# Kernel tuning notes

Hardware: AMD Instinct MI355X
Metric: run time of the kernel (lower is better)

## Reference

```python
import jax, jax.numpy as jnp
import numpy as np

N_BLOCKS = 500000
BLOCK_DIM = 64


def setup_inputs() -> dict:
    key = jax.random.key(0)
    ks = jax.random.split(key, 7)
    d = BLOCK_DIM
    s = jax.random.normal(ks[0], (d,), dtype=jnp.float32)
    h = jax.random.normal(ks[1], (N_BLOCKS * d,), dtype=jnp.float32)
    keys = jax.random.normal(ks[2], (N_BLOCKS, d), dtype=jnp.float32)
    # xavier-uniform style scale for d x d matrices
    lim = np.sqrt(6.0 / (d + d)).astype(np.float32)
    U = jax.random.uniform(ks[3], (d, d), dtype=jnp.float32, minval=-lim, maxval=lim)
    V = jax.random.uniform(ks[4], (d, d), dtype=jnp.float32, minval=-lim, maxval=lim)
    W = jax.random.uniform(ks[5], (d, d), dtype=jnp.float32, minval=-lim, maxval=lim)
    bias = jnp.full((d,), 0.001, dtype=jnp.float32)
    prelu_a = jnp.array([0.25], dtype=jnp.float32)  # nn.PReLU() default
    return {"s": s, "h": h, "keys": keys, "U": U, "V": V, "W": W,
            "bias": bias, "prelu_a": prelu_a}


def reference(s, h, keys, U, V, W, bias, prelu_a):
    d = s.shape[0]
    hb = h.reshape(-1, d)                      # [N, d] blocks of h
    # gate: sigmoid(<s,hj> + <s,wj>) per block
    g = jax.nn.sigmoid(hb @ s + keys @ s)      # [N]
    # candidate: PReLU(U hj + V wj + W s + b), batched over blocks
    pre = hb @ U.T + keys @ V.T + (W @ s) + bias  # [N, d]
    act = jnp.where(pre >= 0, pre, prelu_a[0] * pre)
    h_new = hb + g[:, None] * act              # gated residual update
    h_new = h_new / jnp.linalg.norm(h_new, axis=1, keepdims=True)
    return h_new.reshape(-1)
```

## Files before the change

kernel.cpp:

```cpp
#include <hip/hip_runtime.h>

#define D 64
#define ROWS 64
#define TPB 256

typedef float f4 __attribute__((ext_vector_type(4)));
typedef short s8 __attribute__((ext_vector_type(8)));

static __device__ __forceinline__ unsigned short f2bf(float x) {
  union { float f; unsigned u; } v; v.f = x;
  return (unsigned short)((v.u + 0x7FFFu + ((v.u >> 16) & 1u)) >> 16);
}

static __device__ __forceinline__ s8 pack8(f4 a, f4 b) {
  s8 r;
  r[0] = (short)f2bf(a.x); r[1] = (short)f2bf(a.y);
  r[2] = (short)f2bf(a.z); r[3] = (short)f2bf(a.w);
  r[4] = (short)f2bf(b.x); r[5] = (short)f2bf(b.y);
  r[6] = (short)f2bf(b.z); r[7] = (short)f2bf(b.w);
  return r;
}

static __device__ __forceinline__ f4 fma4s(float a, f4 b, f4 c) {
  f4 r;
  r.x = fmaf(a, b.x, c.x);
  r.y = fmaf(a, b.y, c.y);
  r.z = fmaf(a, b.z, c.z);
  r.w = fmaf(a, b.w, c.w);
  return r;
}

static __device__ __forceinline__ f4 prelu4(f4 p, float a) {
  f4 r;
  r.x = p.x >= 0.0f ? p.x : a * p.x;
  r.y = p.y >= 0.0f ? p.y : a * p.y;
  r.z = p.z >= 0.0f ? p.z : a * p.z;
  r.w = p.w >= 0.0f ? p.w : a * p.w;
  return r;
}

static __device__ __forceinline__ float dot4(f4 x, f4 y, f4 z, float acc) {
  acc = fmaf(x.x + y.x, z.x, acc);
  acc = fmaf(x.y + y.y, z.y, acc);
  acc = fmaf(x.z + y.z, z.z, acc);
  acc = fmaf(x.w + y.w, z.w, acc);
  return acc;
}

__global__ __launch_bounds__(TPB, 4) void dmc_fused(
    const float* __restrict__ h,
    const float* __restrict__ keys,
    const float* __restrict__ s,
    const float* __restrict__ U,
    const float* __restrict__ V,
    const float* __restrict__ W,
    const float* __restrict__ bias,
    const float* __restrict__ prelu_a,
    float* __restrict__ out,
    const int nblocks) {
  __shared__ __align__(16) unsigned short Ub[D * D];
  __shared__ __align__(16) unsigned short Vb[D * D];
  __shared__ __align__(16) float cc[D];

  const int tid  = threadIdx.x;
  const int lane = tid & 63;
  const int wv   = tid >> 6;
  const int j0   = blockIdx.x * ROWS;
  const int nrem = nblocks - j0;

  const f4* __restrict__ Ug = reinterpret_cast<const f4*>(U);
  const f4* __restrict__ Vg = reinterpret_cast<const f4*>(V);
  s8* __restrict__ Ub8w = reinterpret_cast<s8*>(Ub);
  s8* __restrict__ Vb8w = reinterpret_cast<s8*>(Vb);
  #pragma unroll
  for (int t = 0; t < 2; ++t) {
    const int m  = tid + TPB * t;
    const int c  = m >> 3;
    const int sl = m & 7;
    Ub8w[c * 8 + (sl ^ (c & 7))] = pack8(Ug[c * 16 + sl * 2], Ug[c * 16 + sl * 2 + 1]);
    Vb8w[c * 8 + (sl ^ (c & 7))] = pack8(Vg[c * 16 + sl * 2], Vg[c * 16 + sl * 2 + 1]);
  }

  if (tid < D) {
    const f4* __restrict__ wr = reinterpret_cast<const f4*>(W + tid * D);
    const f4* __restrict__ sr = reinterpret_cast<const f4*>(s);
    float acc = bias[tid];
    #pragma unroll
    for (int q = 0; q < 16; ++q) {
      const f4 wq = wr[q];
      const f4 sq = sr[q];
      acc = fmaf(wq.x, sq.x, acc);
      acc = fmaf(wq.y, sq.y, acc);
      acc = fmaf(wq.z, sq.z, acc);
      acc = fmaf(wq.w, sq.w, acc);
    }
    cc[tid] = acc;
  }
  __syncthreads();

  const int g  = lane >> 4;
  const int rl = lane & 15;
  const int r  = wv * 16 + rl;
  const int rc = (r < nrem) ? r : (nrem - 1);

  const f4* __restrict__ hrow = reinterpret_cast<const f4*>(h + (size_t)(j0 + rc) * D);
  const f4* __restrict__ krow = reinterpret_cast<const f4*>(keys + (size_t)(j0 + rc) * D);
  const f4* __restrict__ sg4  = reinterpret_cast<const f4*>(s);

  const f4 h0a = hrow[2 * g];      const f4 h0b = hrow[2 * g + 1];
  const f4 h1a = hrow[8 + 2 * g];  const f4 h1b = hrow[8 + 2 * g + 1];
  const f4 k0a = krow[2 * g];      const f4 k0b = krow[2 * g + 1];
  const f4 k1a = krow[8 + 2 * g];  const f4 k1b = krow[8 + 2 * g + 1];

  float gd = 0.0f;
  gd = dot4(h0a, k0a, sg4[2 * g], gd);
  gd = dot4(h0b, k0b, sg4[2 * g + 1], gd);
  gd = dot4(h1a, k1a, sg4[8 + 2 * g], gd);
  gd = dot4(h1b, k1b, sg4[8 + 2 * g + 1], gd);

  const s8 bh0 = pack8(h0a, h0b);
  const s8 bh1 = pack8(h1a, h1b);
  const s8 bk0 = pack8(k0a, k0b);
  const s8 bk1 = pack8(k1a, k1b);

  const f4* __restrict__ cc4 = reinterpret_cast<const f4*>(cc);
  f4 acc0 = cc4[0 + g];
  f4 acc1 = cc4[4 + g];
  f4 acc2 = cc4[8 + g];
  f4 acc3 = cc4[12 + g];

  const s8* __restrict__ Ub8 = reinterpret_cast<const s8*>(Ub);
  const s8* __restrict__ Vb8 = reinterpret_cast<const s8*>(Vb);
  #pragma unroll
  for (int ks = 0; ks < 2; ++ks) {
    const int asl = ks * 4 + g;
    const s8 bh = (ks == 0) ? bh0 : bh1;
    const s8 bk = (ks == 0) ? bk0 : bk1;
    const int c0i = 0 * 16 + rl, c1i = 1 * 16 + rl;
    const int c2i = 2 * 16 + rl, c3i = 3 * 16 + rl;
    const s8 au0 = Ub8[c0i * 8 + (asl ^ (c0i & 7))];
    const s8 au1 = Ub8[c1i * 8 + (asl ^ (c1i & 7))];
    const s8 au2 = Ub8[c2i * 8 + (asl ^ (c2i & 7))];
    const s8 au3 = Ub8[c3i * 8 + (asl ^ (c3i & 7))];
    const s8 av0 = Vb8[c0i * 8 + (asl ^ (c0i & 7))];
    const s8 av1 = Vb8[c1i * 8 + (asl ^ (c1i & 7))];
    const s8 av2 = Vb8[c2i * 8 + (asl ^ (c2i & 7))];
    const s8 av3 = Vb8[c3i * 8 + (asl ^ (c3i & 7))];
    acc0 = __builtin_amdgcn_mfma_f32_16x16x32_bf16(au0, bh, acc0, 0, 0, 0);
    acc1 = __builtin_amdgcn_mfma_f32_16x16x32_bf16(au1, bh, acc1, 0, 0, 0);
    acc2 = __builtin_amdgcn_mfma_f32_16x16x32_bf16(au2, bh, acc2, 0, 0, 0);
    acc3 = __builtin_amdgcn_mfma_f32_16x16x32_bf16(au3, bh, acc3, 0, 0, 0);
    acc0 = __builtin_amdgcn_mfma_f32_16x16x32_bf16(av0, bk, acc0, 0, 0, 0);
    acc1 = __builtin_amdgcn_mfma_f32_16x16x32_bf16(av1, bk, acc1, 0, 0, 0);
    acc2 = __builtin_amdgcn_mfma_f32_16x16x32_bf16(av2, bk, acc2, 0, 0, 0);
    acc3 = __builtin_amdgcn_mfma_f32_16x16x32_bf16(av3, bk, acc3, 0, 0, 0);
  }

  gd += __shfl_xor(gd, 16);
  gd += __shfl_xor(gd, 32);
  const float gt = 1.0f / (1.0f + __expf(-gd));
  const float a  = prelu_a[0];

  const f4 hr0 = hrow[0 + g];
  const f4 hr1 = hrow[4 + g];
  const f4 hr2 = hrow[8 + g];
  const f4 hr3 = hrow[12 + g];
  f4 o0 = fma4s(gt, prelu4(acc0, a), hr0);
  f4 o1 = fma4s(gt, prelu4(acc1, a), hr1);
  f4 o2 = fma4s(gt, prelu4(acc2, a), hr2);
  f4 o3 = fma4s(gt, prelu4(acc3, a), hr3);

  float ss = o0.x * o0.x + o0.y * o0.y + o0.z * o0.z + o0.w * o0.w;
  ss = fmaf(o1.x, o1.x, ss); ss = fmaf(o1.y, o1.y, ss);
  ss = fmaf(o1.z, o1.z, ss); ss = fmaf(o1.w, o1.w, ss);
  ss = fmaf(o2.x, o2.x, ss); ss = fmaf(o2.y, o2.y, ss);
  ss = fmaf(o2.z, o2.z, ss); ss = fmaf(o2.w, o2.w, ss);
  ss = fmaf(o3.x, o3.x, ss); ss = fmaf(o3.y, o3.y, ss);
  ss = fmaf(o3.z, o3.z, ss); ss = fmaf(o3.w, o3.w, ss);
  ss += __shfl_xor(ss, 16);
  ss += __shfl_xor(ss, 32);
  const float rn = rsqrtf(ss);

  if (r < nrem) {
    float* __restrict__ orow = out + (size_t)(j0 + r) * D + g * 4;
    *reinterpret_cast<f4*>(orow +  0) = o0 * rn;
    *reinterpret_cast<f4*>(orow + 16) = o1 * rn;
    *reinterpret_cast<f4*>(orow + 32) = o2 * rn;
    *reinterpret_cast<f4*>(orow + 48) = o3 * rn;
  }
}

extern "C" void kernel_launch(void* const* d_in, const int* in_sizes, int n_in,
                              void* d_out, int out_size, void* d_ws, size_t ws_size,
                              hipStream_t stream) {
  const float* s       = (const float*)d_in[0];
  const float* h       = (const float*)d_in[1];
  const float* keys    = (const float*)d_in[2];
  const float* U       = (const float*)d_in[3];
  const float* V       = (const float*)d_in[4];
  const float* W       = (const float*)d_in[5];
  const float* bias    = (const float*)d_in[6];
  const float* prelu_a = (const float*)d_in[7];
  float* out = (float*)d_out;

  const int nblocks = in_sizes[1] / D;
  const int grid = (nblocks + ROWS - 1) / ROWS;
  dmc_fused<<<grid, TPB, 0, stream>>>(h, keys, s, U, V, W, bias, prelu_a, out,
                                      nblocks);
}
```

Baseline: 112.4 us.

## Convert to persistent grid-stride kernel with register prefetch of next tile

The one-tile-per-block launch becomes a persistent kernel capped at 768 blocks, each looping over tiles in grid-stride order. Each block converts U/V to bf16 in LDS and computes W·s+bias only once, instead of once per tile. Inside the loop, the h/keys rows for the next tile are loaded into registers while the current tile's MFMAs and epilogue run, to hide global memory latency. Launch bounds drop to 3 waves per SIMD to leave room for the extra prefetch registers, which may reduce occupancy.

```diff
diff --git a/kernel.cpp b/kernel.cpp
--- a/kernel.cpp
+++ b/kernel.cpp
@@ -47,7 +47,7 @@
   return acc;
 }
 
-__global__ __launch_bounds__(TPB, 4) void dmc_fused(
+__global__ __launch_bounds__(TPB, 3) void dmc_fused(
     const float* __restrict__ h,
     const float* __restrict__ keys,
     const float* __restrict__ s,
@@ -57,7 +57,8 @@
     const float* __restrict__ bias,
     const float* __restrict__ prelu_a,
     float* __restrict__ out,
-    const int nblocks) {
+    const int nblocks,
+    const int ntiles) {
   __shared__ __align__(16) unsigned short Ub[D * D];
   __shared__ __align__(16) unsigned short Vb[D * D];
   __shared__ __align__(16) float cc[D];
@@ -65,8 +66,9 @@
   const int tid  = threadIdx.x;
   const int lane = tid & 63;
   const int wv   = tid >> 6;
-  const int j0   = blockIdx.x * ROWS;
-  const int nrem = nblocks - j0;
+  const int g    = lane >> 4;
+  const int rl   = lane & 15;
+  const int r    = wv * 16 + rl;
 
   const f4* __restrict__ Ug = reinterpret_cast<const f4*>(U);
   const f4* __restrict__ Vg = reinterpret_cast<const f4*>(V);
@@ -96,97 +98,124 @@
     }
     cc[tid] = acc;
   }
+
+  const f4* __restrict__ sg4 = reinterpret_cast<const f4*>(s);
+  const f4 sA0 = sg4[2 * g];
+  const f4 sA1 = sg4[2 * g + 1];
+  const f4 sB0 = sg4[8 + 2 * g];
+  const f4 sB1 = sg4[8 + 2 * g + 1];
+  const float a = prelu_a[0];
+
+  int tt = blockIdx.x;
+  f4 ph0a, ph0b, ph1a, ph1b, pk0a, pk0b, pk1a, pk1b;
+  {
+    const int j0 = tt * ROWS;
+    const int nrem = nblocks - j0;
+    const int rc = (r < nrem) ? r : (nrem - 1);
+    const f4* __restrict__ hrow = reinterpret_cast<const f4*>(h + (size_t)(j0 + rc) * D);
+    const f4* __restrict__ krow = reinterpret_cast<const f4*>(keys + (size_t)(j0 + rc) * D);
+    ph0a = hrow[2 * g];     ph0b = hrow[2 * g + 1];
+    ph1a = hrow[8 + 2 * g]; ph1b = hrow[8 + 2 * g + 1];
+    pk0a = krow[2 * g];     pk0b = krow[2 * g + 1];
+    pk1a = krow[8 + 2 * g]; pk1b = krow[8 + 2 * g + 1];
+  }
+
   __syncthreads();
 
-  const int g  = lane >> 4;
-  const int rl = lane & 15;
-  const int r  = wv * 16 + rl;
-  const int rc = (r < nrem) ? r : (nrem - 1);
-
-  const f4* __restrict__ hrow = reinterpret_cast<const f4*>(h + (size_t)(j0 + rc) * D);
-  const f4* __restrict__ krow = reinterpret_cast<const f4*>(keys + (size_t)(j0 + rc) * D);
-  const f4* __restrict__ sg4  = reinterpret_cast<const f4*>(s);
-
-  const f4 h0a = hrow[2 * g];      const f4 h0b = hrow[2 * g + 1];
-  const f4 h1a = hrow[8 + 2 * g];  const f4 h1b = hrow[8 + 2 * g + 1];
-  const f4 k0a = krow[2 * g];      const f4 k0b = krow[2 * g + 1];
-  const f4 k1a = krow[8 + 2 * g];  const f4 k1b = krow[8 + 2 * g + 1];
-
-  float gd = 0.0f;
-  gd = dot4(h0a, k0a, sg4[2 * g], gd);
-  gd = dot4(h0b, k0b, sg4[2 * g + 1], gd);
-  gd = dot4(h1a, k1a, sg4[8 + 2 * g], gd);
-  gd = dot4(h1b, k1b, sg4[8 + 2 * g + 1], gd);
-
-  const s8 bh0 = pack8(h0a, h0b);
-  const s8 bh1 = pack8(h1a, h1b);
-  const s8 bk0 = pack8(k0a, k0b);
-  const s8 bk1 = pack8(k1a, k1b);
-
   const f4* __restrict__ cc4 = reinterpret_cast<const f4*>(cc);
-  f4 acc0 = cc4[0 + g];
-  f4 acc1 = cc4[4 + g];
-  f4 acc2 = cc4[8 + g];
-  f4 acc3 = cc4[12 + g];
+  const f4 ci0 = cc4[0 + g];
+  const f4 ci1 = cc4[4 + g];
+  const f4 ci2 = cc4[8 + g];
+  const f4 ci3 = cc4[12 + g];
 
   const s8* __restrict__ Ub8 = reinterpret_cast<const s8*>(Ub);
   const s8* __restrict__ Vb8 = reinterpret_cast<const s8*>(Vb);
-  #pragma unroll
-  for (int ks = 0; ks < 2; ++ks) {
-    const int asl = ks * 4 + g;
-    const s8 bh = (ks == 0) ? bh0 : bh1;
-    const s8 bk = (ks == 0) ? bk0 : bk1;
-    const int c0i = 0 * 16 + rl, c1i = 1 * 16 + rl;
-    const int c2i = 2 * 16 + rl, c3i = 3 * 16 + rl;
-    const s8 au0 = Ub8[c0i * 8 + (asl ^ (c0i & 7))];
-    const s8 au1 = Ub8[c1i * 8 + (asl ^ (c1i & 7))];
-    const s8 au2 = Ub8[c2i * 8 + (asl ^ (c2i & 7))];
-    const s8 au3 = Ub8[c3i * 8 + (asl ^ (c3i & 7))];
-    const s8 av0 = Vb8[c0i * 8 + (asl ^ (c0i & 7))];
-    const s8 av1 = Vb8[c1i * 8 + (asl ^ (c1i & 7))];
-    const s8 av2 = Vb8[c2i * 8 + (asl ^ (c2i & 7))];
-    const s8 av3 = Vb8[c3i * 8 + (asl ^ (c3i & 7))];
-    acc0 = __builtin_amdgcn_mfma_f32_16x16x32_bf16(au0, bh, acc0, 0, 0, 0);
-    acc1 = __builtin_amdgcn_mfma_f32_16x16x32_bf16(au1, bh, acc1, 0, 0, 0);
-    acc2 = __builtin_amdgcn_mfma_f32_16x16x32_bf16(au2, bh, acc2, 0, 0, 0);
-    acc3 = __builtin_amdgcn_mfma_f32_16x16x32_bf16(au3, bh, acc3, 0, 0, 0);
-    acc0 = __builtin_amdgcn_mfma_f32_16x16x32_bf16(av0, bk, acc0, 0, 0, 0);
-    acc1 = __builtin_amdgcn_mfma_f32_16x16x32_bf16(av1, bk, acc1, 0, 0, 0);
-    acc2 = __builtin_amdgcn_mfma_f32_16x16x32_bf16(av2, bk, acc2, 0, 0, 0);
-    acc3 = __builtin_amdgcn_mfma_f32_16x16x32_bf16(av3, bk, acc3, 0, 0, 0);
-  }
-
-  gd += __shfl_xor(gd, 16);
-  gd += __shfl_xor(gd, 32);
-  const float gt = 1.0f / (1.0f + __expf(-gd));
-  const float a  = prelu_a[0];
-
-  const f4 hr0 = hrow[0 + g];
-  const f4 hr1 = hrow[4 + g];
-  const f4 hr2 = hrow[8 + g];
-  const f4 hr3 = hrow[12 + g];
-  f4 o0 = fma4s(gt, prelu4(acc0, a), hr0);
-  f4 o1 = fma4s(gt, prelu4(acc1, a), hr1);
-  f4 o2 = fma4s(gt, prelu4(acc2, a), hr2);
-  f4 o3 = fma4s(gt, prelu4(acc3, a), hr3);
-
-  float ss = o0.x * o0.x + o0.y * o0.y + o0.z * o0.z + o0.w * o0.w;
-  ss = fmaf(o1.x, o1.x, ss); ss = fmaf(o1.y, o1.y, ss);
-  ss = fmaf(o1.z, o1.z, ss); ss = fmaf(o1.w, o1.w, ss);
-  ss = fmaf(o2.x, o2.x, ss); ss = fmaf(o2.y, o2.y, ss);
-  ss = fmaf(o2.z, o2.z, ss); ss = fmaf(o2.w, o2.w, ss);
-  ss = fmaf(o3.x, o3.x, ss); ss = fmaf(o3.y, o3.y, ss);
-  ss = fmaf(o3.z, o3.z, ss); ss = fmaf(o3.w, o3.w, ss);
-  ss += __shfl_xor(ss, 16);
-  ss += __shfl_xor(ss, 32);
-  const float rn = rsqrtf(ss);
-
-  if (r < nrem) {
-    float* __restrict__ orow = out + (size_t)(j0 + r) * D + g * 4;
-    *reinterpret_cast<f4*>(orow +  0) = o0 * rn;
-    *reinterpret_cast<f4*>(orow + 16) = o1 * rn;
-    *reinterpret_cast<f4*>(orow + 32) = o2 * rn;
-    *reinterpret_cast<f4*>(orow + 48) = o3 * rn;
+  const int xr = rl & 7;
+  const int iu0 = (rl) * 8,      iu1 = (16 + rl) * 8;
+  const int iu2 = (32 + rl) * 8, iu3 = (48 + rl) * 8;
+  const int slA = (0 + g) ^ xr;
+  const int slB = (4 + g) ^ xr;
+
+  while (tt < ntiles) {
+    const int ct = tt;
+    tt += gridDim.x;
+    const int j0   = ct * ROWS;
+    const int nrem = nblocks - j0;
+    const int rc   = (r < nrem) ? r : (nrem - 1);
+    const float* __restrict__ hrowp = h + (size_t)(j0 + rc) * D;
+
+    float gd = dot4(ph0a, pk0a, sA0, 0.0f);
+    gd = dot4(ph0b, pk0b, sA1, gd);
+    gd = dot4(ph1a, pk1a, sB0, gd);
+    gd = dot4(ph1b, pk1b, sB1, gd);
+    const s8 bh0 = pack8(ph0a, ph0b);
+    const s8 bh1 = pack8(ph1a, ph1b);
+    const s8 bk0 = pack8(pk0a, pk0b);
+    const s8 bk1 = pack8(pk1a, pk1b);
+
+    const f4* __restrict__ hrow4 = reinterpret_cast<const f4*>(hrowp);
+    const f4 hr0 = hrow4[0 + g];
+    const f4 hr1 = hrow4[4 + g];
+    const f4 hr2 = hrow4[8 + g];
+    const f4 hr3 = hrow4[12 + g];
+
+    if (tt < ntiles) {
+      const int j0n = tt * ROWS;
+      const int nremn = nblocks - j0n;
+      const int rcn = (r < nremn) ? r : (nremn - 1);
+      const f4* __restrict__ hrn = reinterpret_cast<const f4*>(h + (size_t)(j0n + rcn) * D);
+      const f4* __restrict__ krn = reinterpret_cast<const f4*>(keys + (size_t)(j0n + rcn) * D);
+      ph0a = hrn[2 * g];     ph0b = hrn[2 * g + 1];
+      ph1a = hrn[8 + 2 * g]; ph1b = hrn[8 + 2 * g + 1];
+      pk0a = krn[2 * g];     pk0b = krn[2 * g + 1];
+      pk1a = krn[8 + 2 * g]; pk1b = krn[8 + 2 * g + 1];
+    }
+
+    f4 a0 = ci0, a1 = ci1, a2 = ci2, a3 = ci3;
+    a0 = __builtin_amdgcn_mfma_f32_16x16x32_bf16(Ub8[iu0 + slA], bh0, a0, 0, 0, 0);
+    a1 = __builtin_amdgcn_mfma_f32_16x16x32_bf16(Ub8[iu1 + slA], bh0, a1, 0, 0, 0);
+    a2 = __builtin_amdgcn_mfma_f32_16x16x32_bf16(Ub8[iu2 + slA], bh0, a2, 0, 0, 0);
+    a3 = __builtin_amdgcn_mfma_f32_16x16x32_bf16(Ub8[iu3 + slA], bh0, a3, 0, 0, 0);
+    a0 = __builtin_amdgcn_mfma_f32_16x16x32_bf16(Vb8[iu0 + slA], bk0, a0, 0, 0, 0);
+    a1 = __builtin_amdgcn_mfma_f32_16x16x32_bf16(Vb8[iu1 + slA], bk0, a1, 0, 0, 0);
+    a2 = __builtin_amdgcn_mfma_f32_16x16x32_bf16(Vb8[iu2 + slA], bk0, a2, 0, 0, 0);
+    a3 = __builtin_amdgcn_mfma_f32_16x16x32_bf16(Vb8[iu3 + slA], bk0, a3, 0, 0, 0);
+    a0 = __builtin_amdgcn_mfma_f32_16x16x32_bf16(Ub8[iu0 + slB], bh1, a0, 0, 0, 0);
+    a1 = __builtin_amdgcn_mfma_f32_16x16x32_bf16(Ub8[iu1 + slB], bh1, a1, 0, 0, 0);
+    a2 = __builtin_amdgcn_mfma_f32_16x16x32_bf16(Ub8[iu2 + slB], bh1, a2, 0, 0, 0);
+    a3 = __builtin_amdgcn_mfma_f32_16x16x32_bf16(Ub8[iu3 + slB], bh1, a3, 0, 0, 0);
+    a0 = __builtin_amdgcn_mfma_f32_16x16x32_bf16(Vb8[iu0 + slB], bk1, a0, 0, 0, 0);
+    a1 = __builtin_amdgcn_mfma_f32_16x16x32_bf16(Vb8[iu1 + slB], bk1, a1, 0, 0, 0);
+    a2 = __builtin_amdgcn_mfma_f32_16x16x32_bf16(Vb8[iu2 + slB], bk1, a2, 0, 0, 0);
+    a3 = __builtin_amdgcn_mfma_f32_16x16x32_bf16(Vb8[iu3 + slB], bk1, a3, 0, 0, 0);
+
+    gd += __shfl_xor(gd, 16);
+    gd += __shfl_xor(gd, 32);
+    const float gt = 1.0f / (1.0f + __expf(-gd));
+
+    f4 o0 = fma4s(gt, prelu4(a0, a), hr0);
+    f4 o1 = fma4s(gt, prelu4(a1, a), hr1);
+    f4 o2 = fma4s(gt, prelu4(a2, a), hr2);
+    f4 o3 = fma4s(gt, prelu4(a3, a), hr3);
+
+    float ss = o0.x * o0.x + o0.y * o0.y + o0.z * o0.z + o0.w * o0.w;
+    ss = fmaf(o1.x, o1.x, ss); ss = fmaf(o1.y, o1.y, ss);
+    ss = fmaf(o1.z, o1.z, ss); ss = fmaf(o1.w, o1.w, ss);
+    ss = fmaf(o2.x, o2.x, ss); ss = fmaf(o2.y, o2.y, ss);
+    ss = fmaf(o2.z, o2.z, ss); ss = fmaf(o2.w, o2.w, ss);
+    ss = fmaf(o3.x, o3.x, ss); ss = fmaf(o3.y, o3.y, ss);
+    ss = fmaf(o3.z, o3.z, ss); ss = fmaf(o3.w, o3.w, ss);
+    ss += __shfl_xor(ss, 16);
+    ss += __shfl_xor(ss, 32);
+    const float rn = rsqrtf(ss);
+
+    if (r < nrem) {
+      float* __restrict__ orow = out + (size_t)(j0 + r) * D + g * 4;
+      *reinterpret_cast<f4*>(orow +  0) = o0 * rn;
+      *reinterpret_cast<f4*>(orow + 16) = o1 * rn;
+      *reinterpret_cast<f4*>(orow + 32) = o2 * rn;
+      *reinterpret_cast<f4*>(orow + 48) = o3 * rn;
+    }
   }
 }
 
@@ -204,7 +233,8 @@
   float* out = (float*)d_out;
 
   const int nblocks = in_sizes[1] / D;
-  const int grid = (nblocks + ROWS - 1) / ROWS;
+  const int ntiles  = (nblocks + ROWS - 1) / ROWS;
+  const int grid    = (ntiles < 768) ? ntiles : 768;
   dmc_fused<<<grid, TPB, 0, stream>>>(h, keys, s, U, V, W, bias, prelu_a, out,
-                                      nblocks);
-}
+                                      nblocks, ntiles);
+}
```

After: 132.2 us. +17.7%, slower.
